# Kernel tuning notes

Measured on AMD Instinct MI355X. Metric: run time of the kernel, lower is better.

Reference implementation:

```python
import jax, jax.numpy as jnp
import numpy as np

NUM_MAPS = 512
NUM_BLOCKS = 2
ZG = 512
HID = min(96, NUM_MAPS)          # shared query / attention hidden dim
SEQ = 8                           # hardcoded inner sequence length
H1 = min(NUM_MAPS // 32, 3)       # num_heads1 = 3
H2 = NUM_MAPS // 32               # num_heads2 = 16
NPROC = NUM_BLOCKS * 4            # 4 FiLM param types per block


def _mha(q, k, v, nheads):
    """Multi-head attention. q:(Lq,D) k,v:(Lk,D) -> (Lq,D)."""
    Lq, D = q.shape
    Lk = k.shape[0]
    d = D // nheads
    qh = q.reshape(Lq, nheads, d).transpose(1, 0, 2)   # (h,Lq,d)
    kh = k.reshape(Lk, nheads, d).transpose(1, 0, 2)
    vh = v.reshape(Lk, nheads, d).transpose(1, 0, 2)
    A = jax.nn.softmax(jnp.einsum('hqd,hkd->hqk', qh, kh) / jnp.sqrt(jnp.asarray(D, q.dtype)))
    O = jnp.einsum('hqk,hkd->hqd', A, vh)
    return O.transpose(1, 0, 2).reshape(Lq, D)


def setup_inputs() -> dict:
    key = jax.random.key(0)
    ks = jax.random.split(key, 20)
    s = 0.05
    n = jax.random.normal
    return {
        'gate': jax.random.uniform(ks[0], (1, SEQ), dtype=jnp.float32),
        'x': n(ks[1], (1, ZG), dtype=jnp.float32),
        # shared_layer_alphaC : Linear(ZG, NUM_MAPS) + Sigmoid
        'Wa': n(ks[2], (ZG, NUM_MAPS)) * s, 'ba': jnp.zeros((NUM_MAPS,)),
        # shared_layer_Query : Linear(ZG, HID) + ReLU
        'Wqr': n(ks[3], (ZG, HID)) * s, 'bqr': jnp.zeros((HID,)),
        # stacked FiLM params: [block, {g1,b1,g2,b2}, num_maps, 8]
        'P': n(ks[4], (NUM_BLOCKS, 4, NUM_MAPS, SEQ)) * 0.2,
        'De': n(ks[5], (NUM_BLOCKS, 4, NUM_MAPS, SEQ)) * 0.01,
        'regs': n(ks[6], (NUM_BLOCKS, 4, NUM_MAPS)) * 0.001,
        # SMAB_small processor weights, stacked over the 8 processors
        'Wq1': n(ks[7], (NPROC, NUM_MAPS, HID)) * s,
        'Wk1': n(ks[8], (NPROC, NUM_MAPS, HID)) * s,
        'Wv1': n(ks[9], (NPROC, NUM_MAPS, HID)) * s,
        'fc1': n(ks[10], (NPROC, HID, HID)) * s,
        'Wq2': n(ks[11], (NPROC, HID, HID)) * s,
        'Wk2': n(ks[12], (NPROC, HID, HID)) * s,
        'Wv2': n(ks[13], (NPROC, HID, HID)) * s,
        'fc2': n(ks[14], (NPROC, HID, HID)) * s,
        'Wo': n(ks[15], (NPROC, HID, NUM_MAPS)) * s,
    }


def reference(gate, x, Wa, ba, Wqr, bqr, P, De, regs,
              Wq1, Wk1, Wv1, fc1, Wq2, Wk2, Wv2, fc2, Wo):
    alpha = jax.nn.sigmoid(x @ Wa + ba).reshape(-1)        # (NUM_MAPS,)
    q = jax.nn.relu(x @ Wqr + bqr)                          # (1, HID)

    # per-processor key/value set: transpose(1,0).view(1,8,num_maps)
    K_all = P.reshape(NPROC, NUM_MAPS, SEQ).transpose(0, 2, 1)  # (8procs, 8, NUM_MAPS)

    def smab(K, wq1, wk1, wv1, f1, wq2, wk2, wv2, f2, wo):
        # stage 1: self-attention over the 8-element set (num_heads1)
        Qk = K @ wq1                                        # (8, HID)
        H = Qk + _mha(Qk, K @ wk1, K @ wv1, H1)
        H = H + jax.nn.relu(H @ f1)
        # stage 2: task query attends to the set (num_heads2)
        Qq = q @ wq2                                        # (1, HID)
        O = Qq + _mha(Qq, H @ wk2, H @ wv2, H2)
        O = O + jax.nn.relu(O @ f2)
        return (O @ wo)[0]                                  # (NUM_MAPS,)

    trans = jax.vmap(smab)(K_all, Wq1, Wk1, Wv1, fc1, Wq2, Wk2, Wv2, fc2, Wo)
    trans = trans.reshape(NUM_BLOCKS, 4, NUM_MAPS)

    de = (De * gate[0]).sum(-1)                             # (NB,4,NUM_MAPS)
    mix = alpha * trans + (1.0 - alpha) * de
    offs = jnp.array([1.0, 0.0, 1.0, 0.0], dtype=mix.dtype).reshape(1, 4, 1)
    # gamma gets +1 offset, beta does not
    return mix * regs + offs
```

## Files before the change

### kernel.cpp

```cpp
#include <hip/hip_runtime.h>
#include <hip/hip_bf16.h>
#include <math.h>


#define WS_ALPHA 0
#define WS_Q     512
#define WS_QKV   608
#define WS_K2    19040
#define WS_V2    25184

__global__ __launch_bounds__(256) void kA_qkv_alpha_q(
    const float* __restrict__ x, const float* __restrict__ Wa,
    const float* __restrict__ ba, const float* __restrict__ Wqr,
    const float* __restrict__ bqr, const float* __restrict__ P,
    const float* __restrict__ Wq1, const float* __restrict__ Wk1,
    const float* __restrict__ Wv1, float* __restrict__ ws)
{
    __shared__ float sK[8 * 528];
    __shared__ float sp[2048];
    const int blk = blockIdx.x, tid = threadIdx.x;

    if (blk < 144) {
        const int proc = blk / 18, rem = blk % 18, mat = rem / 6, six = rem % 6;
        const float4* P4 = (const float4*)(P + proc * 4096);
        for (int i = tid; i < 1024; i += 256) {
            float4 v = P4[i];
            const int c = i >> 1, off = (i & 1) * 4;
            const int cp = c + (c >> 5);
            sK[(off + 0) * 528 + cp] = v.x;
            sK[(off + 1) * 528 + cp] = v.y;
            sK[(off + 2) * 528 + cp] = v.z;
            sK[(off + 3) * 528 + cp] = v.w;
        }
        __syncthreads();
        const int hl = tid & 15, ks = tid >> 4;
        const int h = six * 16 + hl;
        const float* W = (mat == 0 ? Wq1 : (mat == 1 ? Wk1 : Wv1))
                         + proc * 49152 + (ks * 32) * 96 + h;
        const float* Kb = sK + ks * 33;
        float acc[8] = {0.f,0.f,0.f,0.f,0.f,0.f,0.f,0.f};
        #pragma unroll
        for (int m2 = 0; m2 < 32; ++m2) {
            const float w = W[m2 * 96];
            const float* Kc = Kb + m2;
            #pragma unroll
            for (int s = 0; s < 8; ++s) acc[s] += Kc[s * 528] * w;
        }
        float* spb = sp + ks * 128 + hl * 8;
        #pragma unroll
        for (int s = 0; s < 8; ++s) spb[s] = acc[s];
        __syncthreads();
        if (tid < 128) {
            float a = 0.f;
            #pragma unroll
            for (int u = 0; u < 16; ++u) a += sp[u * 128 + tid];
            const int hl2 = tid >> 3, s = tid & 7;
            ws[WS_QKV + proc * 2304 + mat * 768 + s * 96 + six * 16 + hl2] = a;
        }
    } else if (blk < 176) {
        for (int k = tid; k < 512; k += 256) sK[k] = x[k];
        __syncthreads();
        const int ml = tid & 15, ks = tid >> 4;
        const int m = (blk - 144) * 16 + ml;
        const float* W = Wa + (ks * 32) * 512 + m;
        const float* xq = sK + ks * 32;
        float acc = 0.f;
        #pragma unroll
        for (int k = 0; k < 32; ++k) acc += xq[k] * W[k * 512];
        sp[tid] = acc;
        __syncthreads();
        if (tid < 16) {
            float a = ba[(blk - 144) * 16 + tid];
            #pragma unroll
            for (int u = 0; u < 16; ++u) a += sp[u * 16 + tid];
            ws[WS_ALPHA + (blk - 144) * 16 + tid] = 1.f / (1.f + __expf(-a));
        }
    } else {
        for (int k = tid; k < 512; k += 256) sK[k] = x[k];
        __syncthreads();
        const int hl = tid & 31, ks = tid >> 5;
        const int h = (blk - 176) * 32 + hl;
        const float* W = Wqr + (ks * 64) * 96 + h;
        const float* xq = sK + ks * 64;
        float acc = 0.f;
        #pragma unroll
        for (int k = 0; k < 64; ++k) acc += xq[k] * W[k * 96];
        sp[tid] = acc;
        __syncthreads();
        if (ks == 0) {
            float a = bqr[h];
            #pragma unroll
            for (int u = 0; u < 8; ++u) a += sp[hl + 32 * u];
            ws[WS_Q + h] = fmaxf(a, 0.f);
        }
    }
}

__global__ __launch_bounds__(256) void kB_attn1_fc1_kv2(
    const float* __restrict__ fc1w, const float* __restrict__ Wk2,
    const float* __restrict__ Wv2, float* __restrict__ ws)
{
    const int b = blockIdx.x, proc = b / 6, rem = b % 6;
    const int mat = rem / 3, t = rem % 3, tid = threadIdx.x;
    __shared__ float sQk[768], sKk[768], sVv[768], sH[768], sH2[768], sS[192];
    const float rs = 0.10206207261596577f;

    const float* qkv = ws + WS_QKV + proc * 2304;
    for (int i = tid; i < 768; i += 256) {
        sQk[i] = qkv[i]; sKk[i] = qkv[768 + i]; sVv[i] = qkv[1536 + i];
    }
    __syncthreads();
    if (tid < 192) {
        const int h0 = tid / 64, r64 = tid % 64, si = r64 / 8, sk = r64 % 8;
        float acc = 0.f;
        #pragma unroll
        for (int d = 0; d < 32; ++d)
            acc += sQk[si * 96 + h0 * 32 + d] * sKk[sk * 96 + h0 * 32 + d];
        sS[tid] = acc * rs;
    }
    __syncthreads();
    if (tid < 24) {
        float* row = sS + tid * 8;
        float mx = row[0];
        #pragma unroll
        for (int k = 1; k < 8; ++k) mx = fmaxf(mx, row[k]);
        float e[8], sum = 0.f;
        #pragma unroll
        for (int k = 0; k < 8; ++k) { e[k] = __expf(row[k] - mx); sum += e[k]; }
        const float inv = 1.f / sum;
        #pragma unroll
        for (int k = 0; k < 8; ++k) row[k] = e[k] * inv;
    }
    __syncthreads();
    if (tid < 192) {
        const int h0 = tid / 64, r64 = tid % 64, si = r64 / 8, dq = r64 % 8;
        const float* e = sS + h0 * 64 + si * 8;
        float o0 = 0.f, o1 = 0.f, o2 = 0.f, o3 = 0.f;
        #pragma unroll
        for (int k = 0; k < 8; ++k) {
            const float ek = e[k];
            const float* v = sVv + k * 96 + h0 * 32 + dq * 4;
            o0 += ek * v[0]; o1 += ek * v[1]; o2 += ek * v[2]; o3 += ek * v[3];
        }
        const int base = si * 96 + h0 * 32 + dq * 4;
        sH[base + 0] = sQk[base + 0] + o0;
        sH[base + 1] = sQk[base + 1] + o1;
        sH[base + 2] = sQk[base + 2] + o2;
        sH[base + 3] = sQk[base + 3] + o3;
    }
    __syncthreads();
    #pragma unroll
    for (int r = 0; r < 3; ++r) {
        const int idx = tid + 256 * r, s = idx / 96, j = idx % 96;
        const float* W = fc1w + proc * 9216 + j;
        const float* Hs = sH + s * 96;
        float acc = 0.f;
        #pragma unroll
        for (int i = 0; i < 96; ++i) acc += Hs[i] * W[i * 96];
        sH2[idx] = sH[idx] + fmaxf(acc, 0.f);
    }
    __syncthreads();
    const int s = tid >> 5, jl = tid & 31, j = t * 32 + jl;
    const float* W = (mat ? Wv2 : Wk2) + proc * 9216 + j;
    const float* Hs = sH2 + s * 96;
    float acc = 0.f;
    #pragma unroll
    for (int i = 0; i < 96; ++i) acc += Hs[i] * W[i * 96];
    ws[(mat ? WS_V2 : WS_K2) + proc * 768 + s * 96 + j] = acc;
}

__global__ __launch_bounds__(256) void kC_qq_attn2_fc2_out(
    const float* __restrict__ gate, const float* __restrict__ De,
    const float* __restrict__ regs, const float* __restrict__ Wq2,
    const float* __restrict__ fc2w, const float* __restrict__ Wo,
    const float* __restrict__ ws, float* __restrict__ out)
{
    const int b = blockIdx.x, proc = b >> 3, e = b & 7, tid = threadIdx.x;
    __shared__ float sK2[768], sV2[768];
    __shared__ float sq[96], sQq[96], sO[96], sOf[96], sE2[128], sg[8], sp[256];
    const float rs = 0.10206207261596577f;

    for (int i = tid; i < 768; i += 256) {
        sK2[i] = ws[WS_K2 + proc * 768 + i];
        sV2[i] = ws[WS_V2 + proc * 768 + i];
    }
    if (tid < 96) sq[tid] = ws[WS_Q + tid];
    else if (tid >= 96 && tid < 104) sg[tid - 96] = gate[tid - 96];
    __syncthreads();

    if (tid < 192) {
        const int j = tid % 96, ks = tid / 96;
        const float* W = Wq2 + proc * 9216 + j + (ks * 48) * 96;
        const float* xq = sq + ks * 48;
        float acc = 0.f;
        #pragma unroll
        for (int i = 0; i < 48; ++i) acc += xq[i] * W[i * 96];
        sp[tid] = acc;
    }
    __syncthreads();
    if (tid < 96) sQq[tid] = sp[tid] + sp[96 + tid];
    __syncthreads();

    if (tid < 16) {
        const int h0 = tid;
        float lg[8], mx = -1e30f;
        #pragma unroll
        for (int k = 0; k < 8; ++k) {
            float acc = 0.f;
            #pragma unroll
            for (int d = 0; d < 6; ++d)
                acc += sQq[h0 * 6 + d] * sK2[k * 96 + h0 * 6 + d];
            lg[k] = acc * rs; mx = fmaxf(mx, lg[k]);
        }
        float ex[8], sum = 0.f;
        #pragma unroll
        for (int k = 0; k < 8; ++k) { ex[k] = __expf(lg[k] - mx); sum += ex[k]; }
        const float inv = 1.f / sum;
        #pragma unroll
        for (int k = 0; k < 8; ++k) sE2[h0 * 8 + k] = ex[k] * inv;
    }
    __syncthreads();
    if (tid < 96) {
        const int h0 = tid / 6;
        float o = 0.f;
        #pragma unroll
        for (int k = 0; k < 8; ++k) o += sE2[h0 * 8 + k] * sV2[k * 96 + tid];
        sO[tid] = sQq[tid] + o;
    }
    __syncthreads();
    if (tid < 192) {
        const int j = tid % 96, ks = tid / 96;
        const float* W = fc2w + proc * 9216 + j + (ks * 48) * 96;
        const float* Os = sO + ks * 48;
        float acc = 0.f;
        #pragma unroll
        for (int i = 0; i < 48; ++i) acc += Os[i] * W[i * 96];
        sp[tid] = acc;
    }
    __syncthreads();
    if (tid < 96) sOf[tid] = sO[tid] + fmaxf(sp[tid] + sp[96 + tid], 0.f);
    __syncthreads();

    const int ml = tid & 63, ks = tid >> 6;
    const int m = 64 * e + ml;
    const float* W = Wo + proc * 49152 + m;
    float acc = 0.f;
    #pragma unroll
    for (int i = 0; i < 24; ++i)
        acc += sOf[24 * ks + i] * W[(24 * ks + i) * 512];
    sp[tid] = acc;
    __syncthreads();
    if (ks == 0) {
        const float tr = sp[ml] + sp[ml + 64] + sp[ml + 128] + sp[ml + 192];
        const float4* Dp4 = (const float4*)(De + proc * 4096 + m * 8);
        const float4 d0 = Dp4[0], d1 = Dp4[1];
        const float de = d0.x * sg[0] + d0.y * sg[1] + d0.z * sg[2] + d0.w * sg[3]
                       + d1.x * sg[4] + d1.y * sg[5] + d1.z * sg[6] + d1.w * sg[7];
        const float a = ws[WS_ALPHA + m];
        const float mix = a * tr + (1.f - a) * de;
        const int pt = proc & 3;
        const float off = (pt == 0 || pt == 2) ? 1.f : 0.f;
        out[proc * 512 + m] = mix * regs[proc * 512 + m] + off;
    }
}

extern "C" void kernel_launch(void* const* d_in, const int* in_sizes, int n_in,
                              void* d_out, int out_size, void* d_ws, size_t ws_size,
                              hipStream_t stream)
{
    const float* gate = (const float*)d_in[0];
    const float* x    = (const float*)d_in[1];
    const float* Wa   = (const float*)d_in[2];
    const float* ba   = (const float*)d_in[3];
    const float* Wqr  = (const float*)d_in[4];
    const float* bqr  = (const float*)d_in[5];
    const float* P    = (const float*)d_in[6];
    const float* De   = (const float*)d_in[7];
    const float* regs = (const float*)d_in[8];
    const float* Wq1  = (const float*)d_in[9];
    const float* Wk1  = (const float*)d_in[10];
    const float* Wv1  = (const float*)d_in[11];
    const float* fc1  = (const float*)d_in[12];
    const float* Wq2  = (const float*)d_in[13];
    const float* Wk2  = (const float*)d_in[14];
    const float* Wv2  = (const float*)d_in[15];
    const float* fc2  = (const float*)d_in[16];
    const float* Wo   = (const float*)d_in[17];
    float* ws = (float*)d_ws;

    hipLaunchKernelGGL(kA_qkv_alpha_q, dim3(179), dim3(256), 0, stream,
                       x, Wa, ba, Wqr, bqr, P, Wq1, Wk1, Wv1, ws);
    hipLaunchKernelGGL(kB_attn1_fc1_kv2, dim3(48), dim3(256), 0, stream,
                       fc1, Wk2, Wv2, ws);
    hipLaunchKernelGGL(kC_qq_attn2_fc2_out, dim3(64), dim3(256), 0, stream,
                       gate, De, regs, Wq2, fc2, Wo, ws, (float*)d_out);
}
```

Before: 109.8 us.

## Prefetch weights into registers/LDS up front and move Qq projection into kernel B

Weight loads in all three kernels are now issued at the start, before the barrier-heavy compute phases. They go into registers in kernel A and as bulk float4 copies into shared memory in kernels B and C, so global-memory latency overlaps the activation staging instead of sitting on the serial dependency chain. The task-query projection (q @ Wq2) moves from kernel C into 24 extra blocks of kernel B, shortening C's critical path. The Wqr path in kernel A is re-split into 16-wide blocks with 32-row chunks, which takes 6 blocks instead of 3. The cost is much larger shared-memory footprints (about 50KB in kernel B), more registers, and extra blocks, any of which could lower occupancy.

```diff
diff --git a/kernel.cpp b/kernel.cpp
--- a/kernel.cpp
+++ b/kernel.cpp
@@ -8,6 +8,7 @@
 #define WS_QKV   608
 #define WS_K2    19040
 #define WS_V2    25184
+#define WS_QQ    31328
 
 __global__ __launch_bounds__(256) void kA_qkv_alpha_q(
     const float* __restrict__ x, const float* __restrict__ Wa,
@@ -22,6 +23,13 @@
 
     if (blk < 144) {
         const int proc = blk / 18, rem = blk % 18, mat = rem / 6, six = rem % 6;
+        const int hl = tid & 15, ks = tid >> 4;
+        const int h = six * 16 + hl;
+        const float* W = (mat == 0 ? Wq1 : (mat == 1 ? Wk1 : Wv1))
+                         + proc * 49152 + (ks * 32) * 96 + h;
+        float wreg[32];
+        #pragma unroll
+        for (int m2 = 0; m2 < 32; ++m2) wreg[m2] = W[m2 * 96];
         const float4* P4 = (const float4*)(P + proc * 4096);
         for (int i = tid; i < 1024; i += 256) {
             float4 v = P4[i];
@@ -33,15 +41,11 @@
             sK[(off + 3) * 528 + cp] = v.w;
         }
         __syncthreads();
-        const int hl = tid & 15, ks = tid >> 4;
-        const int h = six * 16 + hl;
-        const float* W = (mat == 0 ? Wq1 : (mat == 1 ? Wk1 : Wv1))
-                         + proc * 49152 + (ks * 32) * 96 + h;
         const float* Kb = sK + ks * 33;
         float acc[8] = {0.f,0.f,0.f,0.f,0.f,0.f,0.f,0.f};
         #pragma unroll
         for (int m2 = 0; m2 < 32; ++m2) {
-            const float w = W[m2 * 96];
+            const float w = wreg[m2];
             const float* Kc = Kb + m2;
             #pragma unroll
             for (int s = 0; s < 8; ++s) acc[s] += Kc[s * 528] * w;
@@ -58,15 +62,18 @@
             ws[WS_QKV + proc * 2304 + mat * 768 + s * 96 + six * 16 + hl2] = a;
         }
     } else if (blk < 176) {
-        for (int k = tid; k < 512; k += 256) sK[k] = x[k];
-        __syncthreads();
         const int ml = tid & 15, ks = tid >> 4;
         const int m = (blk - 144) * 16 + ml;
         const float* W = Wa + (ks * 32) * 512 + m;
+        float wreg[32];
+        #pragma unroll
+        for (int k = 0; k < 32; ++k) wreg[k] = W[k * 512];
+        for (int k = tid; k < 512; k += 256) sK[k] = x[k];
+        __syncthreads();
         const float* xq = sK + ks * 32;
         float acc = 0.f;
         #pragma unroll
-        for (int k = 0; k < 32; ++k) acc += xq[k] * W[k * 512];
+        for (int k = 0; k < 32; ++k) acc += xq[k] * wreg[k];
         sp[tid] = acc;
         __syncthreads();
         if (tid < 16) {
@@ -76,129 +83,178 @@
             ws[WS_ALPHA + (blk - 144) * 16 + tid] = 1.f / (1.f + __expf(-a));
         }
     } else {
+        const int hl = tid & 15, ks = tid >> 4;
+        const int h = (blk - 176) * 16 + hl;
+        const float* W = Wqr + (ks * 32) * 96 + h;
+        float wreg[32];
+        #pragma unroll
+        for (int k = 0; k < 32; ++k) wreg[k] = W[k * 96];
         for (int k = tid; k < 512; k += 256) sK[k] = x[k];
         __syncthreads();
-        const int hl = tid & 31, ks = tid >> 5;
-        const int h = (blk - 176) * 32 + hl;
-        const float* W = Wqr + (ks * 64) * 96 + h;
-        const float* xq = sK + ks * 64;
-        float acc = 0.f;
-        #pragma unroll
-        for (int k = 0; k < 64; ++k) acc += xq[k] * W[k * 96];
+        const float* xq = sK + ks * 32;
+        float acc = 0.f;
+        #pragma unroll
+        for (int k = 0; k < 32; ++k) acc += xq[k] * wreg[k];
         sp[tid] = acc;
         __syncthreads();
-        if (ks == 0) {
-            float a = bqr[h];
-            #pragma unroll
-            for (int u = 0; u < 8; ++u) a += sp[hl + 32 * u];
-            ws[WS_Q + h] = fmaxf(a, 0.f);
+        if (tid < 16) {
+            float a = bqr[(blk - 176) * 16 + tid];
+            #pragma unroll
+            for (int u = 0; u < 16; ++u) a += sp[u * 16 + tid];
+            ws[WS_Q + (blk - 176) * 16 + tid] = fmaxf(a, 0.f);
         }
     }
 }
 
 __global__ __launch_bounds__(256) void kB_attn1_fc1_kv2(
     const float* __restrict__ fc1w, const float* __restrict__ Wk2,
-    const float* __restrict__ Wv2, float* __restrict__ ws)
+    const float* __restrict__ Wv2, const float* __restrict__ Wq2,
+    float* __restrict__ ws)
 {
-    const int b = blockIdx.x, proc = b / 6, rem = b % 6;
-    const int mat = rem / 3, t = rem % 3, tid = threadIdx.x;
-    __shared__ float sQk[768], sKk[768], sVv[768], sH[768], sH2[768], sS[192];
+    const int b = blockIdx.x, tid = threadIdx.x;
     const float rs = 0.10206207261596577f;
 
-    const float* qkv = ws + WS_QKV + proc * 2304;
-    for (int i = tid; i < 768; i += 256) {
-        sQk[i] = qkv[i]; sKk[i] = qkv[768 + i]; sVv[i] = qkv[1536 + i];
-    }
-    __syncthreads();
-    if (tid < 192) {
-        const int h0 = tid / 64, r64 = tid % 64, si = r64 / 8, sk = r64 % 8;
-        float acc = 0.f;
-        #pragma unroll
-        for (int d = 0; d < 32; ++d)
-            acc += sQk[si * 96 + h0 * 32 + d] * sKk[sk * 96 + h0 * 32 + d];
-        sS[tid] = acc * rs;
-    }
-    __syncthreads();
-    if (tid < 24) {
-        float* row = sS + tid * 8;
-        float mx = row[0];
-        #pragma unroll
-        for (int k = 1; k < 8; ++k) mx = fmaxf(mx, row[k]);
-        float e[8], sum = 0.f;
-        #pragma unroll
-        for (int k = 0; k < 8; ++k) { e[k] = __expf(row[k] - mx); sum += e[k]; }
-        const float inv = 1.f / sum;
-        #pragma unroll
-        for (int k = 0; k < 8; ++k) row[k] = e[k] * inv;
-    }
-    __syncthreads();
-    if (tid < 192) {
-        const int h0 = tid / 64, r64 = tid % 64, si = r64 / 8, dq = r64 % 8;
-        const float* e = sS + h0 * 64 + si * 8;
-        float o0 = 0.f, o1 = 0.f, o2 = 0.f, o3 = 0.f;
-        #pragma unroll
-        for (int k = 0; k < 8; ++k) {
-            const float ek = e[k];
-            const float* v = sVv + k * 96 + h0 * 32 + dq * 4;
-            o0 += ek * v[0]; o1 += ek * v[1]; o2 += ek * v[2]; o3 += ek * v[3];
-        }
-        const int base = si * 96 + h0 * 32 + dq * 4;
-        sH[base + 0] = sQk[base + 0] + o0;
-        sH[base + 1] = sQk[base + 1] + o1;
-        sH[base + 2] = sQk[base + 2] + o2;
-        sH[base + 3] = sQk[base + 3] + o3;
-    }
-    __syncthreads();
-    #pragma unroll
-    for (int r = 0; r < 3; ++r) {
-        const int idx = tid + 256 * r, s = idx / 96, j = idx % 96;
-        const float* W = fc1w + proc * 9216 + j;
-        const float* Hs = sH + s * 96;
-        float acc = 0.f;
-        #pragma unroll
-        for (int i = 0; i < 96; ++i) acc += Hs[i] * W[i * 96];
-        sH2[idx] = sH[idx] + fmaxf(acc, 0.f);
-    }
-    __syncthreads();
-    const int s = tid >> 5, jl = tid & 31, j = t * 32 + jl;
-    const float* W = (mat ? Wv2 : Wk2) + proc * 9216 + j;
-    const float* Hs = sH2 + s * 96;
-    float acc = 0.f;
-    #pragma unroll
-    for (int i = 0; i < 96; ++i) acc += Hs[i] * W[i * 96];
-    ws[(mat ? WS_V2 : WS_K2) + proc * 768 + s * 96 + j] = acc;
+    if (b < 48) {
+        const int proc = b / 6, rem = b % 6, mat = rem / 3, t = rem % 3;
+        __shared__ float sQk[768], sKk[768], sVv[768], sH[768], sH2[768], sS[192];
+        __shared__ float sWf1[9216];
+        __shared__ float sWkv[96 * 32];
+
+        {
+            const float4* F4 = (const float4*)fc1w + proc * 2304;
+            float4* D4 = (float4*)sWf1;
+            #pragma unroll
+            for (int r = 0; r < 9; ++r) D4[tid + 256 * r] = F4[tid + 256 * r];
+            const float4* KV4 = (const float4*)(mat ? Wv2 : Wk2);
+            float4* E4 = (float4*)sWkv;
+            #pragma unroll
+            for (int r = 0; r < 3; ++r) {
+                const int idx = tid + 256 * r;
+                const int row = idx >> 3, q4 = idx & 7;
+                E4[row * 8 + q4] = KV4[proc * 2304 + row * 24 + t * 8 + q4];
+            }
+        }
+        const float* qkv = ws + WS_QKV + proc * 2304;
+        for (int i = tid; i < 768; i += 256) {
+            sQk[i] = qkv[i]; sKk[i] = qkv[768 + i]; sVv[i] = qkv[1536 + i];
+        }
+        __syncthreads();
+
+        if (tid < 192) {
+            const int h0 = tid / 64, r64 = tid % 64, si = r64 / 8, sk = r64 % 8;
+            float acc = 0.f;
+            #pragma unroll
+            for (int d = 0; d < 32; ++d)
+                acc += sQk[si * 96 + h0 * 32 + d] * sKk[sk * 96 + h0 * 32 + d];
+            sS[tid] = acc * rs;
+        }
+        __syncthreads();
+        if (tid < 24) {
+            float* row = sS + tid * 8;
+            float mx = row[0];
+            #pragma unroll
+            for (int k = 1; k < 8; ++k) mx = fmaxf(mx, row[k]);
+            float e[8], sum = 0.f;
+            #pragma unroll
+            for (int k = 0; k < 8; ++k) { e[k] = __expf(row[k] - mx); sum += e[k]; }
+            const float inv = 1.f / sum;
+            #pragma unroll
+            for (int k = 0; k < 8; ++k) row[k] = e[k] * inv;
+        }
+        __syncthreads();
+        if (tid < 192) {
+            const int h0 = tid / 64, r64 = tid % 64, si = r64 / 8, dq = r64 % 8;
+            const float* e = sS + h0 * 64 + si * 8;
+            float o0 = 0.f, o1 = 0.f, o2 = 0.f, o3 = 0.f;
+            #pragma unroll
+            for (int k = 0; k < 8; ++k) {
+                const float ek = e[k];
+                const float* v = sVv + k * 96 + h0 * 32 + dq * 4;
+                o0 += ek*v[0]; o1 += ek*v[1]; o2 += ek*v[2]; o3 += ek*v[3];
+            }
+            const int base = si * 96 + h0 * 32 + dq * 4;
+            sH[base+0] = sQk[base+0] + o0;  sH[base+1] = sQk[base+1] + o1;
+            sH[base+2] = sQk[base+2] + o2;  sH[base+3] = sQk[base+3] + o3;
+        }
+        __syncthreads();
+        #pragma unroll
+        for (int r = 0; r < 3; ++r) {
+            const int idx = tid + 256 * r, s = idx / 96, j = idx % 96;
+            const float* Hs = sH + s * 96;
+            float acc = 0.f;
+            #pragma unroll
+            for (int i = 0; i < 96; ++i) acc += Hs[i] * sWf1[i * 96 + j];
+            sH2[idx] = sH[idx] + fmaxf(acc, 0.f);
+        }
+        __syncthreads();
+        const int s = tid >> 5, jl = tid & 31, j = t * 32 + jl;
+        const float* Hs = sH2 + s * 96;
+        float acc = 0.f;
+        #pragma unroll
+        for (int i = 0; i < 96; ++i) acc += Hs[i] * sWkv[i * 32 + jl];
+        ws[(mat ? WS_V2 : WS_K2) + proc * 768 + s * 96 + j] = acc;
+    } else {
+        const int b2 = b - 48, proc = b2 / 3, t = b2 % 3;
+        __shared__ float sq[96], sp[256];
+        if (tid < 96) sq[tid] = ws[WS_Q + tid];
+        __syncthreads();
+        const int jl = tid & 31, ks = tid >> 5;
+        const int j = 32 * t + jl;
+        const float* W = Wq2 + proc * 9216 + j;
+        float acc = 0.f;
+        #pragma unroll
+        for (int i = 0; i < 12; ++i)
+            acc += sq[12 * ks + i] * W[(12 * ks + i) * 96];
+        sp[tid] = acc;
+        __syncthreads();
+        if (ks == 0) {
+            float a = 0.f;
+            #pragma unroll
+            for (int u = 0; u < 8; ++u) a += sp[jl + 32 * u];
+            ws[WS_QQ + proc * 96 + j] = a;
+        }
+    }
 }
 
-__global__ __launch_bounds__(256) void kC_qq_attn2_fc2_out(
+__global__ __launch_bounds__(256) void kC_attn2_fc2_out(
     const float* __restrict__ gate, const float* __restrict__ De,
-    const float* __restrict__ regs, const float* __restrict__ Wq2,
-    const float* __restrict__ fc2w, const float* __restrict__ Wo,
-    const float* __restrict__ ws, float* __restrict__ out)
+    const float* __restrict__ regs, const float* __restrict__ fc2w,
+    const float* __restrict__ Wo, const float* __restrict__ ws,
+    float* __restrict__ out)
 {
     const int b = blockIdx.x, proc = b >> 3, e = b & 7, tid = threadIdx.x;
     __shared__ float sK2[768], sV2[768];
-    __shared__ float sq[96], sQq[96], sO[96], sOf[96], sE2[128], sg[8], sp[256];
+    __shared__ float sQq[96], sO[96], sOf[96], sE2[128], sg[8], sp[256];
+    __shared__ float sWf2[9216];
+    __shared__ float sWo[96 * 64];
     const float rs = 0.10206207261596577f;
 
+    {
+        const float4* F4 = (const float4*)fc2w + proc * 2304;
+        float4* D4 = (float4*)sWf2;
+        #pragma unroll
+        for (int r = 0; r < 9; ++r) D4[tid + 256 * r] = F4[tid + 256 * r];
+        const float4* W4 = (const float4*)Wo;
+        float4* E4 = (float4*)sWo;
+        #pragma unroll
+        for (int r = 0; r < 6; ++r) {
+            const int idx = tid + 256 * r;
+            const int row = idx >> 4, q4 = idx & 15;
+            E4[row * 16 + q4] = W4[proc * 12288 + row * 128 + e * 16 + q4];
+        }
+    }
+    const int ml = tid & 63, ks = tid >> 6;
+    const int m = 64 * e + ml;
+    const float4* Dp4 = (const float4*)(De + proc * 4096 + m * 8);
+    const float4 d0 = Dp4[0], d1 = Dp4[1];
+    const float av = ws[WS_ALPHA + m];
+    const float rg = regs[proc * 512 + m];
     for (int i = tid; i < 768; i += 256) {
         sK2[i] = ws[WS_K2 + proc * 768 + i];
         sV2[i] = ws[WS_V2 + proc * 768 + i];
     }
-    if (tid < 96) sq[tid] = ws[WS_Q + tid];
+    if (tid < 96) sQq[tid] = ws[WS_QQ + proc * 96 + tid];
     else if (tid >= 96 && tid < 104) sg[tid - 96] = gate[tid - 96];
-    __syncthreads();
-
-    if (tid < 192) {
-        const int j = tid % 96, ks = tid / 96;
-        const float* W = Wq2 + proc * 9216 + j + (ks * 48) * 96;
-        const float* xq = sq + ks * 48;
-        float acc = 0.f;
-        #pragma unroll
-        for (int i = 0; i < 48; ++i) acc += xq[i] * W[i * 96];
-        sp[tid] = acc;
-    }
-    __syncthreads();
-    if (tid < 96) sQq[tid] = sp[tid] + sp[96 + tid];
     __syncthreads();
 
     if (tid < 16) {
@@ -229,38 +285,31 @@
     }
     __syncthreads();
     if (tid < 192) {
-        const int j = tid % 96, ks = tid / 96;
-        const float* W = fc2w + proc * 9216 + j + (ks * 48) * 96;
-        const float* Os = sO + ks * 48;
-        float acc = 0.f;
-        #pragma unroll
-        for (int i = 0; i < 48; ++i) acc += Os[i] * W[i * 96];
+        const int j = tid % 96, k2 = tid / 96;
+        const float* Os = sO + k2 * 48;
+        float acc = 0.f;
+        #pragma unroll
+        for (int i = 0; i < 48; ++i) acc += Os[i] * sWf2[(k2 * 48 + i) * 96 + j];
         sp[tid] = acc;
     }
     __syncthreads();
     if (tid < 96) sOf[tid] = sO[tid] + fmaxf(sp[tid] + sp[96 + tid], 0.f);
     __syncthreads();
 
-    const int ml = tid & 63, ks = tid >> 6;
-    const int m = 64 * e + ml;
-    const float* W = Wo + proc * 49152 + m;
     float acc = 0.f;
     #pragma unroll
     for (int i = 0; i < 24; ++i)
-        acc += sOf[24 * ks + i] * W[(24 * ks + i) * 512];
+        acc += sOf[24 * ks + i] * sWo[(24 * ks + i) * 64 + ml];
     sp[tid] = acc;
     __syncthreads();
     if (ks == 0) {
         const float tr = sp[ml] + sp[ml + 64] + sp[ml + 128] + sp[ml + 192];
-        const float4* Dp4 = (const float4*)(De + proc * 4096 + m * 8);
-        const float4 d0 = Dp4[0], d1 = Dp4[1];
         const float de = d0.x * sg[0] + d0.y * sg[1] + d0.z * sg[2] + d0.w * sg[3]
                        + d1.x * sg[4] + d1.y * sg[5] + d1.z * sg[6] + d1.w * sg[7];
-        const float a = ws[WS_ALPHA + m];
-        const float mix = a * tr + (1.f - a) * de;
+        const float mix = av * tr + (1.f - av) * de;
         const int pt = proc & 3;
         const float off = (pt == 0 || pt == 2) ? 1.f : 0.f;
-        out[proc * 512 + m] = mix * regs[proc * 512 + m] + off;
+        out[proc * 512 + m] = mix * rg + off;
     }
 }
 
@@ -288,10 +337,10 @@
     const float* Wo   = (const float*)d_in[17];
     float* ws = (float*)d_ws;
 
-    hipLaunchKernelGGL(kA_qkv_alpha_q, dim3(179), dim3(256), 0, stream,
+    hipLaunchKernelGGL(kA_qkv_alpha_q, dim3(182), dim3(256), 0, stream,
                        x, Wa, ba, Wqr, bqr, P, Wq1, Wk1, Wv1, ws);
-    hipLaunchKernelGGL(kB_attn1_fc1_kv2, dim3(48), dim3(256), 0, stream,
-                       fc1, Wk2, Wv2, ws);
-    hipLaunchKernelGGL(kC_qq_attn2_fc2_out, dim3(64), dim3(256), 0, stream,
-                       gate, De, regs, Wq2, fc2, Wo, ws, (float*)d_out);
+    hipLaunchKernelGGL(kB_attn1_fc1_kv2, dim3(72), dim3(256), 0, stream,
+                       fc1, Wk2, Wv2, Wq2, ws);
+    hipLaunchKernelGGL(kC_attn2_fc2_out, dim3(64), dim3(256), 0, stream,
+                       gate, De, regs, fc2, Wo, ws, (float*)d_out);
 }
```

Measured after the change: 109.2 us (median of 2 runs). Within noise of the previous version (-0.6%).
